# Kernel optimization log

Measured on AMD Instinct MI355X. Metric: run time of the kernel, lower is better.

## Reference

```python
import jax, jax.numpy as jnp
import numpy as np

B, S, E = 8, 2048, 256
NQ = 10
FF = 1024


def _cnot(state, c, t, n):
    # state: [T, 2^n]; wire 0 is the most-significant bit.
    T = state.shape[0]
    s = state.reshape((T,) + (2,) * n)
    ctrl0 = jnp.take(s, 0, axis=c + 1)
    ctrl1 = jnp.take(s, 1, axis=c + 1)
    # target axis index after removing the control axis
    t_ax = t + 1 if (t + 1) < (c + 1) else t
    ctrl1 = jnp.flip(ctrl1, axis=t_ax)  # X on target where control==1
    s = jnp.stack([ctrl0, ctrl1], axis=c + 1)
    return s.reshape(T, -1)


def _quantum_layer(tok, theta, n):
    # tok: [T, E] real; uses first n features as RX angles. Returns [T, n] PauliZ expvals.
    T = tok.shape[0]
    half = tok[:, :n] * 0.5
    c = jnp.cos(half).astype(jnp.complex64)
    s = (-1j * jnp.sin(half)).astype(jnp.complex64)
    # RX(theta)|0> = cos(t/2)|0> - i sin(t/2)|1>; build product state wire-by-wire
    state = jnp.ones((T, 1), dtype=jnp.complex64)
    for w in range(n):
        qb = jnp.stack([c[:, w], s[:, w]], axis=1)  # [T, 2]
        state = (state[:, :, None] * qb[:, None, :]).reshape(T, -1)
    # trainable RY per wire
    th = theta * 0.5
    for w in range(n):
        ct, st = jnp.cos(th[w]), jnp.sin(th[w])
        U = jnp.stack([jnp.stack([ct, -st]), jnp.stack([st, ct])]).astype(jnp.complex64)
        sr = state.reshape(T, 2 ** w, 2, -1)
        state = jnp.einsum('ij,tajb->taib', U, sr).reshape(T, -1)
    # CNOT ring
    for cw in range(n - 1):
        state = _cnot(state, cw, cw + 1, n)
    state = _cnot(state, n - 1, 0, n)
    probs = state.real ** 2 + state.imag ** 2  # [T, 2^n]
    idx = jnp.arange(2 ** n)
    bits = (idx[None, :] >> (n - 1 - jnp.arange(n)[:, None])) & 1  # [n, 2^n]
    z = (1.0 - 2.0 * bits).astype(probs.dtype)
    return probs @ z.T  # [T, n]


def setup_inputs() -> dict:
    key = jax.random.key(0)
    ks = jax.random.split(key, 6)
    return {
        'x': jax.random.normal(ks[0], (B, S, E), dtype=jnp.float32),
        'theta': jax.random.normal(ks[1], (NQ,), dtype=jnp.float32),
        'w1': jax.random.normal(ks[2], (FF, NQ), dtype=jnp.float32) * (1.0 / np.sqrt(NQ)),
        'b1': jax.random.normal(ks[3], (FF,), dtype=jnp.float32) * 0.02,
        'w2': jax.random.normal(ks[4], (E, FF), dtype=jnp.float32) * (1.0 / np.sqrt(FF)),
        'b2': jax.random.normal(ks[5], (E,), dtype=jnp.float32) * 0.02,
    }


def reference(x, theta, w1, b1, w2, b2):
    b, s, e = x.shape
    n = theta.shape[0]
    q = _quantum_layer(x.reshape(b * s, e), theta, n).reshape(b, s, n)
    # dropout is identity in eval mode
    h = jax.nn.relu(q @ w1.T + b1)
    return h @ w2.T + b2
```

## Files before the change

kernel.cpp:

```cpp
#include <hip/hip_runtime.h>
#include <hip/hip_bf16.h>
#include <math.h>

typedef __attribute__((ext_vector_type(8))) short bf16x8;
typedef __attribute__((ext_vector_type(4))) float f32x4;

#define T_TOT 16384
#define E_ 256
#define FF_ 1024
#define NQ 10
#define TB 64
#define CH 64
#define NCHUNK (FF_ / CH)
#define HGRAN (TB * CH)

__device__ __forceinline__ unsigned pkbf(float a, float b) {
    __hip_bfloat162 t = __float22bfloat162_rn(make_float2(a, b));
    return *(unsigned*)&t;
}

__global__ __launch_bounds__(256) void ffq_prep(
    const float* __restrict__ w2, const float* __restrict__ w1,
    uint4* __restrict__ w2f, uint4* __restrict__ w1f)
{
    int id = blockIdx.x * 256 + threadIdx.x;
    if (id < 32768) {
        int n  = id >> 7;
        int k0 = (id & 127) * 8;
        const float4* s = (const float4*)(w2 + (size_t)n * FF_ + k0);
        float4 a = s[0], b = s[1];
        uint4 v;
        v.x = pkbf(a.x, a.y);
        v.y = pkbf(a.z, a.w);
        v.z = pkbf(b.x, b.y);
        v.w = pkbf(b.z, b.w);
        int idx = ((k0 >> 5) * 16 + (n >> 4)) * 64 + ((k0 >> 3) & 3) * 16 + (n & 15);
        w2f[idx] = v;
    } else if (id < 32768 + 4096) {
        int id2 = id - 32768;
        int l = id2 & 63, nt = id2 >> 6;
        int n = nt * 16 + (l & 15);
        int g = l >> 4;
        float o[8];
#pragma unroll
        for (int j = 0; j < 8; ++j) {
            int k = g * 8 + j;
            o[j] = (k < NQ) ? w1[n * NQ + k] : 0.f;
        }
        uint4 v;
        v.x = pkbf(o[0], o[1]);
        v.y = pkbf(o[2], o[3]);
        v.z = pkbf(o[4], o[5]);
        v.w = pkbf(o[6], o[7]);
        w1f[id2] = v;
    }
}

__global__ __launch_bounds__(256, 8) void ffq_mfma(
    const float* __restrict__ x, const float* __restrict__ theta,
    const float* __restrict__ b1, const float* __restrict__ b2,
    const bf16x8* __restrict__ w1f, const bf16x8* __restrict__ w2f,
    float* __restrict__ out)
{
    __shared__ unsigned short q_s[4 * 64 * 8];
    __shared__ unsigned short hs[2 * HGRAN];

    const int tid = threadIdx.x;
    const int l   = tid & 63;
    const int wv  = tid >> 6;
    const int lr  = l & 15;
    const int g   = l >> 4;
    const int tb  = (blockIdx.x >> 2) * TB;
    const int nc  = (blockIdx.x & 3) * 4 + wv;

    if (tid < TB) {
        const int t = tb + tid;
        float xv[NQ];
        {
            float4 a = *(const float4*)(x + (size_t)t * E_);
            float4 b = *(const float4*)(x + (size_t)t * E_ + 4);
            float2 c = *(const float2*)(x + (size_t)t * E_ + 8);
            xv[0]=a.x; xv[1]=a.y; xv[2]=a.z; xv[3]=a.w;
            xv[4]=b.x; xv[5]=b.y; xv[6]=b.z; xv[7]=b.w;
            xv[8]=c.x; xv[9]=c.y;
        }
        float mm[NQ];
#pragma unroll
        for (int w = 0; w < NQ; ++w) mm[w] = cosf(theta[w]) * cosf(xv[w]);
        float qv[NQ];
        {
            float p = mm[0];
#pragma unroll
            for (int w = 1; w < NQ; ++w) { p *= mm[w]; qv[w] = p; }
            float p0 = mm[1];
#pragma unroll
            for (int w = 2; w < NQ; ++w) p0 *= mm[w];
            qv[0] = p0;
        }
        uint4 s0, s1;
        s0.x = pkbf(qv[0], qv[1]);
        s0.y = pkbf(qv[2], qv[3]);
        s0.z = pkbf(qv[4], qv[5]);
        s0.w = pkbf(qv[6], qv[7]);
        s1.x = pkbf(qv[8], qv[9]);
        s1.y = 0; s1.z = 0; s1.w = 0;
        int tt = tid >> 4, r = tid & 15;
        uint4* base = (uint4*)q_s + tt * 64;
        base[r]      = s0;
        base[16 + r] = s1;
        base[32 + r] = make_uint4(0, 0, 0, 0);
        base[48 + r] = make_uint4(0, 0, 0, 0);
    }
    __syncthreads();

    f32x4 acc[4];
#pragma unroll
    for (int tt = 0; tt < 4; ++tt) acc[tt] = (f32x4){0.f, 0.f, 0.f, 0.f};

#define H_PHASE(cc, hdst, WF, BBC)                                             \
    {                                                                          \
        bf16x8 qfr[4];                                                         \
        _Pragma("unroll")                                                      \
        for (int tt = 0; tt < 4; ++tt)                                         \
            qfr[tt] = ((const bf16x8*)q_s)[tt * 64 + l];                       \
        const int fl   = wv * 16 + g * 4;                \
        const int gb   = fl >> 5;                       \
        const int sl   = (fl & 31) >> 3;                                       \
        const int sub  = (fl & 7) * 2;                                         \
        _Pragma("unroll")                                                      \
        for (int tt = 0; tt < 4; ++tt) {                                       \
            f32x4 d = __builtin_amdgcn_mfma_f32_16x16x32_bf16(                 \
                    (WF), qfr[tt], (BBC), 0, 0, 0);                            \
            unsigned p0 = pkbf(fmaxf(d[0], 0.f), fmaxf(d[1], 0.f));            \
            unsigned p1 = pkbf(fmaxf(d[2], 0.f), fmaxf(d[3], 0.f));            \
            unsigned byteoff = (unsigned)((tt * 2 + gb) * 64 + lr + 16 * sl)   \
                               * 16u + (unsigned)sub;                          \
            *(uint2*)((char*)(hdst) + byteoff) = make_uint2(p0, p1);           \
        }                                                                      \
    }

#define OUT_STEP(J)                                                            \
    {                                                                          \
        const int kk  = c * 2 + (J);                                           \
        const int kkn = (kk + 1 < 32) ? kk + 1 : 31;                           \
        bf16x8 bn = w2f[(kkn * 16 + nc) * 64 + l];                             \
        bf16x8 af[4];                                                          \
        _Pragma("unroll")                                                      \
        for (int tt = 0; tt < 4; ++tt)                                         \
            af[tt] = hc[(tt * 2 + (J)) * 64 + l];                              \
        _Pragma("unroll")                                                      \
        for (int tt = 0; tt < 4; ++tt)                                         \
            acc[tt] = __builtin_amdgcn_mfma_f32_16x16x32_bf16(                 \
                af[tt], bc, acc[tt], 0, 0, 0);                                 \
        bc = bn;                                                               \
    }

    {
        bf16x8 wf0 = w1f[(0 * 4 + wv) * 64 + l];
        f32x4  bb0 = *(const f32x4*)(b1 + (0 * 4 + wv) * 16 + g * 4);
        H_PHASE(0, hs, wf0, bb0)
    }
    bf16x8 bc = w2f[(0 * 16 + nc) * 64 + l];
    __syncthreads();

    for (int c = 0; c < NCHUNK; ++c) {
        const bf16x8*   hc = (const bf16x8*)(hs + (c & 1) * HGRAN);
        unsigned short* hn = hs + ((c & 1) ^ 1) * HGRAN;

        bf16x8 wfc; f32x4 bbc;
        if (c < NCHUNK - 1) {
            wfc = w1f[((c + 1) * 4 + wv) * 64 + l];
            bbc = *(const f32x4*)(b1 + ((c + 1) * 4 + wv) * 16 + g * 4);
        }

        __builtin_amdgcn_s_setprio(1);
        OUT_STEP(0)
        OUT_STEP(1)
        __builtin_amdgcn_s_setprio(0);

        if (c < NCHUNK - 1) {
            H_PHASE(c + 1, hn, wfc, bbc)
        }
        __syncthreads();
    }
#undef OUT_STEP
#undef H_PHASE

    {
        const int col = nc * 16 + lr;
        const float bbv = b2[col];
#pragma unroll
        for (int tt = 0; tt < 4; ++tt) {
#pragma unroll
            for (int r = 0; r < 4; ++r) {
                int tr = tb + tt * 16 + g * 4 + r;
                out[(size_t)tr * E_ + col] = acc[tt][r] + bbv;
            }
        }
    }
}

extern "C" void kernel_launch(void* const* d_in, const int* in_sizes, int n_in,
                              void* d_out, int out_size, void* d_ws, size_t ws_size,
                              hipStream_t stream) {
    const float* x     = (const float*)d_in[0];
    const float* theta = (const float*)d_in[1];
    const float* w1    = (const float*)d_in[2];
    const float* b1    = (const float*)d_in[3];
    const float* w2    = (const float*)d_in[4];
    const float* b2    = (const float*)d_in[5];
    float* out = (float*)d_out;

    uint4* w2f = (uint4*)d_ws;
    uint4* w1f = (uint4*)((char*)d_ws + 512 * 1024);

    hipLaunchKernelGGL(ffq_prep, dim3(144), dim3(256), 0, stream,
                       w2, w1, w2f, w1f);
    hipLaunchKernelGGL(ffq_mfma, dim3(4 * T_TOT / TB), dim3(256), 0, stream,
                       x, theta, b1, b2,
                       (const bf16x8*)w1f, (const bf16x8*)w2f, out);
}
```

Baseline: 30.69 us.

## Compute all output columns per block with LDS-staged W2 and wider hidden chunks

Each block now covers a 64-token tile across all 256 output columns using 8 waves, with each wave computing two 16-column tiles. Before, four blocks each covered a quarter of the columns and all four recomputed the same hidden activations. W2 fragments are staged through double-buffered shared memory, with register prefetch from global, and the hidden chunk grows to 128. This removes the fourfold redundant hidden-layer compute and the quantum prelude per token, and shares W2 loads across waves. In exchange it uses much more LDS, fewer and larger blocks (256 blocks of 512 threads), lower occupancy, and one extra barrier per W2 pair.

```diff
diff --git a/kernel.cpp b/kernel.cpp
--- a/kernel.cpp
+++ b/kernel.cpp
@@ -10,9 +10,10 @@
 #define FF_ 1024
 #define NQ 10
 #define TB 64
-#define CH 64
+#define CH 128
 #define NCHUNK (FF_ / CH)
 #define HGRAN (TB * CH)
+#define BPAIR (32 * 512)
 
 __device__ __forceinline__ unsigned pkbf(float a, float b) {
     __hip_bfloat162 t = __float22bfloat162_rn(make_float2(a, b));
@@ -56,7 +57,7 @@
     }
 }
 
-__global__ __launch_bounds__(256, 8) void ffq_mfma(
+__global__ __launch_bounds__(512, 2) void ffq_mfma(
     const float* __restrict__ x, const float* __restrict__ theta,
     const float* __restrict__ b1, const float* __restrict__ b2,
     const bf16x8* __restrict__ w1f, const bf16x8* __restrict__ w2f,
@@ -64,14 +65,16 @@
 {
     __shared__ unsigned short q_s[4 * 64 * 8];
     __shared__ unsigned short hs[2 * HGRAN];
+    __shared__ unsigned short Bl[2 * BPAIR];
 
     const int tid = threadIdx.x;
     const int l   = tid & 63;
     const int wv  = tid >> 6;
     const int lr  = l & 15;
     const int g   = l >> 4;
-    const int tb  = (blockIdx.x >> 2) * TB;
-    const int nc  = (blockIdx.x & 3) * 4 + wv;
+    const int tb  = blockIdx.x * TB;
+    const int nc0 = wv * 2;
+    const int nc1 = wv * 2 + 1;
 
     if (tid < TB) {
         const int t = tb + tid;
@@ -111,90 +114,108 @@
         base[32 + r] = make_uint4(0, 0, 0, 0);
         base[48 + r] = make_uint4(0, 0, 0, 0);
     }
-    __syncthreads();
-
-    f32x4 acc[4];
-#pragma unroll
-    for (int tt = 0; tt < 4; ++tt) acc[tt] = (f32x4){0.f, 0.f, 0.f, 0.f};
-
-#define H_PHASE(cc, hdst, WF, BBC)                                             \
+
+    f32x4 acc[4][2];
+#pragma unroll
+    for (int tt = 0; tt < 4; ++tt)
+#pragma unroll
+        for (int nn = 0; nn < 2; ++nn) acc[tt][nn] = (f32x4){0.f,0.f,0.f,0.f};
+
+#define H_PHASE(cc, hdst)                                                      \
     {                                                                          \
+        const int ntg = (cc) * 8 + wv;                                         \
+        bf16x8 wf  = w1f[ntg * 64 + l];                                        \
+        f32x4  bbc = *(const f32x4*)(b1 + ntg * 16 + g * 4);                   \
         bf16x8 qfr[4];                                                         \
         _Pragma("unroll")                                                      \
         for (int tt = 0; tt < 4; ++tt)                                         \
             qfr[tt] = ((const bf16x8*)q_s)[tt * 64 + l];                       \
-        const int fl   = wv * 16 + g * 4;                \
-        const int gb   = fl >> 5;                       \
-        const int sl   = (fl & 31) >> 3;                                       \
-        const int sub  = (fl & 7) * 2;                                         \
+        const int fl  = wv * 16 + g * 4;                 \
+        const int kkl = fl >> 5;                                               \
+        const int sl  = (fl & 31) >> 3;                                        \
+        const int sub = (fl & 7) * 2;                                          \
         _Pragma("unroll")                                                      \
         for (int tt = 0; tt < 4; ++tt) {                                       \
             f32x4 d = __builtin_amdgcn_mfma_f32_16x16x32_bf16(                 \
-                    (WF), qfr[tt], (BBC), 0, 0, 0);                            \
+                    wf, qfr[tt], bbc, 0, 0, 0);                                \
             unsigned p0 = pkbf(fmaxf(d[0], 0.f), fmaxf(d[1], 0.f));            \
             unsigned p1 = pkbf(fmaxf(d[2], 0.f), fmaxf(d[3], 0.f));            \
-            unsigned byteoff = (unsigned)((tt * 2 + gb) * 64 + lr + 16 * sl)   \
+            unsigned byteoff = (unsigned)((tt * 4 + kkl) * 64 + lr + 16 * sl)  \
                                * 16u + (unsigned)sub;                          \
             *(uint2*)((char*)(hdst) + byteoff) = make_uint2(p0, p1);           \
         }                                                                      \
     }
 
-#define OUT_STEP(J)                                                            \
-    {                                                                          \
-        const int kk  = c * 2 + (J);                                           \
-        const int kkn = (kk + 1 < 32) ? kk + 1 : 31;                           \
-        bf16x8 bn = w2f[(kkn * 16 + nc) * 64 + l];                             \
-        bf16x8 af[4];                                                          \
-        _Pragma("unroll")                                                      \
-        for (int tt = 0; tt < 4; ++tt)                                         \
-            af[tt] = hc[(tt * 2 + (J)) * 64 + l];                              \
-        _Pragma("unroll")                                                      \
-        for (int tt = 0; tt < 4; ++tt)                                         \
-            acc[tt] = __builtin_amdgcn_mfma_f32_16x16x32_bf16(                 \
-                af[tt], bc, acc[tt], 0, 0, 0);                                 \
-        bc = bn;                                                               \
-    }
+    bf16x8 stg[4];
+#pragma unroll
+    for (int r = 0; r < 4; ++r)
+        stg[r] = w2f[(0 * 32 + r * 8 + wv) * 64 + l];
+#pragma unroll
+    for (int r = 0; r < 4; ++r)
+        ((bf16x8*)Bl)[(r * 8 + wv) * 64 + l] = stg[r];
+    __syncthreads();
+
+    H_PHASE(0, hs)
+#pragma unroll
+    for (int r = 0; r < 4; ++r)
+        stg[r] = w2f[(1 * 32 + r * 8 + wv) * 64 + l];
+    __syncthreads();
+
+#pragma unroll 2
+    for (int p = 0; p < 16; ++p) {
+        const bf16x8* bcur = (const bf16x8*)(Bl + (p & 1) * BPAIR);
+        bf16x8*       bnxt = (bf16x8*)(Bl + ((p & 1) ^ 1) * BPAIR);
+        const bf16x8* hc   = (const bf16x8*)(hs + ((p >> 1) & 1) * HGRAN);
+
+#pragma unroll
+        for (int e = 0; e < 2; ++e) {
+            const int kkl = ((p & 1) << 1) + e;
+            bf16x8 af[4];
+#pragma unroll
+            for (int tt = 0; tt < 4; ++tt)
+                af[tt] = hc[(tt * 4 + kkl) * 64 + l];
+            bf16x8 b0 = bcur[(e * 16 + nc0) * 64 + l];
+            bf16x8 b1v = bcur[(e * 16 + nc1) * 64 + l];
+#pragma unroll
+            for (int tt = 0; tt < 4; ++tt)
+                acc[tt][0] = __builtin_amdgcn_mfma_f32_16x16x32_bf16(
+                    af[tt], b0, acc[tt][0], 0, 0, 0);
+#pragma unroll
+            for (int tt = 0; tt < 4; ++tt)
+                acc[tt][1] = __builtin_amdgcn_mfma_f32_16x16x32_bf16(
+                    af[tt], b1v, acc[tt][1], 0, 0, 0);
+        }
+
+        if ((p & 1) == 1 && p < 15) {
+            H_PHASE((p >> 1) + 1, hs + (((p >> 1) & 1) ^ 1) * HGRAN)
+        }
+
+        if (p < 15) {
+#pragma unroll
+            for (int r = 0; r < 4; ++r)
+                bnxt[(r * 8 + wv) * 64 + l] = stg[r];
+            if (p < 14) {
+#pragma unroll
+                for (int r = 0; r < 4; ++r)
+                    stg[r] = w2f[((p + 2) * 32 + r * 8 + wv) * 64 + l];
+            }
+        }
+        __syncthreads();
+    }
+#undef H_PHASE
 
     {
-        bf16x8 wf0 = w1f[(0 * 4 + wv) * 64 + l];
-        f32x4  bb0 = *(const f32x4*)(b1 + (0 * 4 + wv) * 16 + g * 4);
-        H_PHASE(0, hs, wf0, bb0)
-    }
-    bf16x8 bc = w2f[(0 * 16 + nc) * 64 + l];
-    __syncthreads();
-
-    for (int c = 0; c < NCHUNK; ++c) {
-        const bf16x8*   hc = (const bf16x8*)(hs + (c & 1) * HGRAN);
-        unsigned short* hn = hs + ((c & 1) ^ 1) * HGRAN;
-
-        bf16x8 wfc; f32x4 bbc;
-        if (c < NCHUNK - 1) {
-            wfc = w1f[((c + 1) * 4 + wv) * 64 + l];
-            bbc = *(const f32x4*)(b1 + ((c + 1) * 4 + wv) * 16 + g * 4);
-        }
-
-        __builtin_amdgcn_s_setprio(1);
-        OUT_STEP(0)
-        OUT_STEP(1)
-        __builtin_amdgcn_s_setprio(0);
-
-        if (c < NCHUNK - 1) {
-            H_PHASE(c + 1, hn, wfc, bbc)
-        }
-        __syncthreads();
-    }
-#undef OUT_STEP
-#undef H_PHASE
-
-    {
-        const int col = nc * 16 + lr;
-        const float bbv = b2[col];
+        const int col0 = nc0 * 16 + lr;
+        const int col1 = col0 + 16;
+        const float bb0 = b2[col0];
+        const float bb1 = b2[col1];
 #pragma unroll
         for (int tt = 0; tt < 4; ++tt) {
 #pragma unroll
             for (int r = 0; r < 4; ++r) {
                 int tr = tb + tt * 16 + g * 4 + r;
-                out[(size_t)tr * E_ + col] = acc[tt][r] + bbv;
+                out[(size_t)tr * E_ + col0] = acc[tt][0][r] + bb0;
+                out[(size_t)tr * E_ + col1] = acc[tt][1][r] + bb1;
             }
         }
     }
@@ -216,7 +237,7 @@
 
     hipLaunchKernelGGL(ffq_prep, dim3(144), dim3(256), 0, stream,
                        w2, w1, w2f, w1f);
-    hipLaunchKernelGGL(ffq_mfma, dim3(4 * T_TOT / TB), dim3(256), 0, stream,
+    hipLaunchKernelGGL(ffq_mfma, dim3(T_TOT / TB), dim3(512), 0, stream,
                        x, theta, b1, b2,
                        (const bf16x8*)w1f, (const bf16x8*)w2f, out);
 }
```

Result: faster. 27.65 us (-9.9%).

## Stage W2 column slice in LDS and loop blocks over multiple token subtiles

Applied to the files above, without the earlier changes.

Each block now loads its 64-column slice of the packed W2 (128 KB) into shared memory once and then processes four 64-token subtiles in a loop. Blocks are 512 threads, split into two token halves and four column groups. The intent is to replace repeated global or L2 reads of W2 per 64-token tile with LDS reads reused across 256 tokens. In exchange the kernel uses a large LDS footprint, which limits occupancy to about one or two blocks per CU. It also launches fewer blocks (256), pays an upfront W2 load per block, and adds more barriers per subtile.

```diff
diff --git a/kernel.cpp b/kernel.cpp
--- a/kernel.cpp
+++ b/kernel.cpp
@@ -9,10 +9,11 @@
 #define E_ 256
 #define FF_ 1024
 #define NQ 10
-#define TB 64
+#define TOKS 256
+#define NSUB 4
 #define CH 64
-#define NCHUNK (FF_ / CH)
-#define HGRAN (TB * CH)
+#define NCH (FF_ / CH)
+#define HG (64 * CH)
 
 __device__ __forceinline__ unsigned pkbf(float a, float b) {
     __hip_bfloat162 t = __float22bfloat162_rn(make_float2(a, b));
@@ -56,145 +57,151 @@
     }
 }
 
-__global__ __launch_bounds__(256, 8) void ffq_mfma(
+__global__ __launch_bounds__(512, 2) void ffq_mfma(
     const float* __restrict__ x, const float* __restrict__ theta,
     const float* __restrict__ b1, const float* __restrict__ b2,
     const bf16x8* __restrict__ w1f, const bf16x8* __restrict__ w2f,
     float* __restrict__ out)
 {
+    __shared__ bf16x8        Bl[8192];
     __shared__ unsigned short q_s[4 * 64 * 8];
-    __shared__ unsigned short hs[2 * HGRAN];
+    __shared__ unsigned short hs[2 * HG];
 
     const int tid = threadIdx.x;
     const int l   = tid & 63;
     const int wv  = tid >> 6;
     const int lr  = l & 15;
     const int g   = l >> 4;
-    const int tb  = (blockIdx.x >> 2) * TB;
-    const int nc  = (blockIdx.x & 3) * 4 + wv;
-
-    if (tid < TB) {
-        const int t = tb + tid;
-        float xv[NQ];
-        {
-            float4 a = *(const float4*)(x + (size_t)t * E_);
-            float4 b = *(const float4*)(x + (size_t)t * E_ + 4);
-            float2 c = *(const float2*)(x + (size_t)t * E_ + 8);
-            xv[0]=a.x; xv[1]=a.y; xv[2]=a.z; xv[3]=a.w;
-            xv[4]=b.x; xv[5]=b.y; xv[6]=b.z; xv[7]=b.w;
-            xv[8]=c.x; xv[9]=c.y;
-        }
-        float mm[NQ];
-#pragma unroll
-        for (int w = 0; w < NQ; ++w) mm[w] = cosf(theta[w]) * cosf(xv[w]);
-        float qv[NQ];
-        {
-            float p = mm[0];
-#pragma unroll
-            for (int w = 1; w < NQ; ++w) { p *= mm[w]; qv[w] = p; }
-            float p0 = mm[1];
-#pragma unroll
-            for (int w = 2; w < NQ; ++w) p0 *= mm[w];
-            qv[0] = p0;
-        }
-        uint4 s0, s1;
-        s0.x = pkbf(qv[0], qv[1]);
-        s0.y = pkbf(qv[2], qv[3]);
-        s0.z = pkbf(qv[4], qv[5]);
-        s0.w = pkbf(qv[6], qv[7]);
-        s1.x = pkbf(qv[8], qv[9]);
-        s1.y = 0; s1.z = 0; s1.w = 0;
-        int tt = tid >> 4, r = tid & 15;
-        uint4* base = (uint4*)q_s + tt * 64;
-        base[r]      = s0;
-        base[16 + r] = s1;
-        base[32 + r] = make_uint4(0, 0, 0, 0);
-        base[48 + r] = make_uint4(0, 0, 0, 0);
+    const int tp  = wv >> 2;
+    const int wc  = wv & 3;
+    const int cb  = blockIdx.x & 3;
+    const int tb  = (blockIdx.x >> 2) * TOKS;
+
+#pragma unroll
+    for (int half = 0; half < 2; ++half) {
+        bf16x8 tmp[8];
+#pragma unroll
+        for (int i = 0; i < 8; ++i) {
+            int e  = (half * 8 + i) * 512 + tid;
+            int kk = e >> 8, wcl = (e >> 6) & 3, ll = e & 63;
+            tmp[i] = w2f[(kk * 16 + cb * 4 + wcl) * 64 + ll];
+        }
+#pragma unroll
+        for (int i = 0; i < 8; ++i) {
+            int e = (half * 8 + i) * 512 + tid;
+            Bl[e] = tmp[i];
+        }
     }
-    __syncthreads();
-
-    f32x4 acc[4];
-#pragma unroll
-    for (int tt = 0; tt < 4; ++tt) acc[tt] = (f32x4){0.f, 0.f, 0.f, 0.f};
-
-#define H_PHASE(cc, hdst, WF, BBC)                                             \
-    {                                                                          \
-        bf16x8 qfr[4];                                                         \
-        _Pragma("unroll")                                                      \
-        for (int tt = 0; tt < 4; ++tt)                                         \
-            qfr[tt] = ((const bf16x8*)q_s)[tt * 64 + l];                       \
-        const int fl   = wv * 16 + g * 4;                \
-        const int gb   = fl >> 5;                       \
-        const int sl   = (fl & 31) >> 3;                                       \
-        const int sub  = (fl & 7) * 2;                                         \
-        _Pragma("unroll")                                                      \
-        for (int tt = 0; tt < 4; ++tt) {                                       \
-            f32x4 d = __builtin_amdgcn_mfma_f32_16x16x32_bf16(                 \
-                    (WF), qfr[tt], (BBC), 0, 0, 0);                            \
-            unsigned p0 = pkbf(fmaxf(d[0], 0.f), fmaxf(d[1], 0.f));            \
-            unsigned p1 = pkbf(fmaxf(d[2], 0.f), fmaxf(d[3], 0.f));            \
-            unsigned byteoff = (unsigned)((tt * 2 + gb) * 64 + lr + 16 * sl)   \
-                               * 16u + (unsigned)sub;                          \
-            *(uint2*)((char*)(hdst) + byteoff) = make_uint2(p0, p1);           \
-        }                                                                      \
-    }
-
-#define OUT_STEP(J)                                                            \
-    {                                                                          \
-        const int kk  = c * 2 + (J);                                           \
-        const int kkn = (kk + 1 < 32) ? kk + 1 : 31;                           \
-        bf16x8 bn = w2f[(kkn * 16 + nc) * 64 + l];                             \
-        bf16x8 af[4];                                                          \
-        _Pragma("unroll")                                                      \
-        for (int tt = 0; tt < 4; ++tt)                                         \
-            af[tt] = hc[(tt * 2 + (J)) * 64 + l];                              \
-        _Pragma("unroll")                                                      \
-        for (int tt = 0; tt < 4; ++tt)                                         \
-            acc[tt] = __builtin_amdgcn_mfma_f32_16x16x32_bf16(                 \
-                af[tt], bc, acc[tt], 0, 0, 0);                                 \
-        bc = bn;                                                               \
-    }
-
-    {
-        bf16x8 wf0 = w1f[(0 * 4 + wv) * 64 + l];
-        f32x4  bb0 = *(const f32x4*)(b1 + (0 * 4 + wv) * 16 + g * 4);
-        H_PHASE(0, hs, wf0, bb0)
-    }
-    bf16x8 bc = w2f[(0 * 16 + nc) * 64 + l];
-    __syncthreads();
-
-    for (int c = 0; c < NCHUNK; ++c) {
-        const bf16x8*   hc = (const bf16x8*)(hs + (c & 1) * HGRAN);
-        unsigned short* hn = hs + ((c & 1) ^ 1) * HGRAN;
-
-        bf16x8 wfc; f32x4 bbc;
-        if (c < NCHUNK - 1) {
-            wfc = w1f[((c + 1) * 4 + wv) * 64 + l];
-            bbc = *(const f32x4*)(b1 + ((c + 1) * 4 + wv) * 16 + g * 4);
-        }
-
-        __builtin_amdgcn_s_setprio(1);
-        OUT_STEP(0)
-        OUT_STEP(1)
-        __builtin_amdgcn_s_setprio(0);
-
-        if (c < NCHUNK - 1) {
-            H_PHASE(c + 1, hn, wfc, bbc)
+
+    const int col  = (cb * 4 + wc) * 16 + lr;
+    const float bbv = b2[col];
+
+    for (int s = 0; s < NSUB; ++s) {
+        if (tid < 64) {
+            const int t = tb + s * 64 + tid;
+            float xv[NQ];
+            {
+                float4 a = *(const float4*)(x + (size_t)t * E_);
+                float4 b = *(const float4*)(x + (size_t)t * E_ + 4);
+                float2 c = *(const float2*)(x + (size_t)t * E_ + 8);
+                xv[0]=a.x; xv[1]=a.y; xv[2]=a.z; xv[3]=a.w;
+                xv[4]=b.x; xv[5]=b.y; xv[6]=b.z; xv[7]=b.w;
+                xv[8]=c.x; xv[9]=c.y;
+            }
+            float mm[NQ];
+#pragma unroll
+            for (int w = 0; w < NQ; ++w) mm[w] = cosf(theta[w]) * cosf(xv[w]);
+            float qv[NQ];
+            {
+                float p = mm[0];
+#pragma unroll
+                for (int w = 1; w < NQ; ++w) { p *= mm[w]; qv[w] = p; }
+                float p0 = mm[1];
+#pragma unroll
+                for (int w = 2; w < NQ; ++w) p0 *= mm[w];
+                qv[0] = p0;
+            }
+            uint4 s0, s1;
+            s0.x = pkbf(qv[0], qv[1]);
+            s0.y = pkbf(qv[2], qv[3]);
+            s0.z = pkbf(qv[4], qv[5]);
+            s0.w = pkbf(qv[6], qv[7]);
+            s1.x = pkbf(qv[8], qv[9]);
+            s1.y = 0; s1.z = 0; s1.w = 0;
+            int tt = tid >> 4, r = tid & 15;
+            uint4* base = (uint4*)q_s + tt * 64;
+            base[r]      = s0;
+            base[16 + r] = s1;
+            base[32 + r] = make_uint4(0, 0, 0, 0);
+            base[48 + r] = make_uint4(0, 0, 0, 0);
         }
         __syncthreads();
-    }
-#undef OUT_STEP
+
+        bf16x8 qfr[2];
+        qfr[0] = ((const bf16x8*)q_s)[(tp * 2 + 0) * 64 + l];
+        qfr[1] = ((const bf16x8*)q_s)[(tp * 2 + 1) * 64 + l];
+
+        f32x4 acc[2];
+        acc[0] = (f32x4){0.f, 0.f, 0.f, 0.f};
+        acc[1] = (f32x4){0.f, 0.f, 0.f, 0.f};
+
+#define H_PHASE(cc, hdst)                                                      \
+        {                                                                      \
+            const int ntg = (cc) * 4 + wc;                                     \
+            bf16x8 wf  = w1f[ntg * 64 + l];                                    \
+            f32x4  bbc = *(const f32x4*)(b1 + ntg * 16 + g * 4);               \
+            const int fl  = wc * 16 + g * 4;          \
+            const int kkl = fl >> 5;                                           \
+            const int sl  = (fl & 31) >> 3;                                    \
+            const int sub = (fl & 7) * 2;                                      \
+            _Pragma("unroll")                                                  \
+            for (int j = 0; j < 2; ++j) {                                      \
+                const int tt = tp * 2 + j;                                     \
+                f32x4 d = __builtin_amdgcn_mfma_f32_16x16x32_bf16(             \
+                        wf, qfr[j], bbc, 0, 0, 0);                             \
+                unsigned p0 = pkbf(fmaxf(d[0], 0.f), fmaxf(d[1], 0.f));        \
+                unsigned p1 = pkbf(fmaxf(d[2], 0.f), fmaxf(d[3], 0.f));        \
+                unsigned byteoff = (unsigned)((tt * 2 + kkl) * 64 + lr         \
+                                   + 16 * sl) * 16u + (unsigned)sub;           \
+                *(uint2*)((char*)(hdst) + byteoff) = make_uint2(p0, p1);       \
+            }                                                                  \
+        }
+
+        H_PHASE(0, hs)
+        __syncthreads();
+
+        for (int c = 0; c < NCH; ++c) {
+            const bf16x8*   hc = (const bf16x8*)(hs + (c & 1) * HG);
+            unsigned short* hn = hs + ((c & 1) ^ 1) * HG;
+
+            __builtin_amdgcn_s_setprio(1);
+#pragma unroll
+            for (int kkl = 0; kkl < 2; ++kkl) {
+                const int kk = c * 2 + kkl;
+                bf16x8 bb  = Bl[(kk * 4 + wc) * 64 + l];
+                bf16x8 af0 = hc[((tp * 2 + 0) * 2 + kkl) * 64 + l];
+                bf16x8 af1 = hc[((tp * 2 + 1) * 2 + kkl) * 64 + l];
+                acc[0] = __builtin_amdgcn_mfma_f32_16x16x32_bf16(
+                    af0, bb, acc[0], 0, 0, 0);
+                acc[1] = __builtin_amdgcn_mfma_f32_16x16x32_bf16(
+                    af1, bb, acc[1], 0, 0, 0);
+            }
+            __builtin_amdgcn_s_setprio(0);
+
+            if (c < NCH - 1) {
+                H_PHASE(c + 1, hn)
+            }
+            __syncthreads();
+        }
 #undef H_PHASE
 
-    {
-        const int col = nc * 16 + lr;
-        const float bbv = b2[col];
-#pragma unroll
-        for (int tt = 0; tt < 4; ++tt) {
+#pragma unroll
+        for (int j = 0; j < 2; ++j) {
+            const int tt = tp * 2 + j;
 #pragma unroll
             for (int r = 0; r < 4; ++r) {
-                int tr = tb + tt * 16 + g * 4 + r;
-                out[(size_t)tr * E_ + col] = acc[tt][r] + bbv;
+                int tr = tb + s * 64 + tt * 16 + g * 4 + r;
+                out[(size_t)tr * E_ + col] = acc[j][r] + bbv;
             }
         }
     }
@@ -216,7 +223,7 @@
 
     hipLaunchKernelGGL(ffq_prep, dim3(144), dim3(256), 0, stream,
                        w2, w1, w2f, w1f);
-    hipLaunchKernelGGL(ffq_mfma, dim3(4 * T_TOT / TB), dim3(256), 0, stream,
+    hipLaunchKernelGGL(ffq_mfma, dim3(T_TOT / TOKS * 4), dim3(512), 0, stream,
                        x, theta, b1, b2,
                        (const bf16x8*)w1f, (const bf16x8*)w2f, out);
 }
```

Result: slower. 52.23 us (+70.2%).
